# Optimization experiments

Hardware: AMD Instinct MI355X
Metric: run time of the kernel (lower is better)

## Reference

```python
import jax, jax.numpy as jnp
import numpy as np

D = 1024
T = 32768


def setup_inputs() -> dict:
    key = jax.random.key(0)
    k1, k2, k3 = jax.random.split(key, 3)
    r_star = jax.random.normal(k1, (D,), dtype=jnp.float32)
    q_t = jax.random.normal(k2, (T, D), dtype=jnp.float32)
    W = jax.random.normal(k3, (D,), dtype=jnp.float32) * (2.0 / D) ** 0.5  # ~GlorotNormal
    b = jnp.zeros((1,), dtype=jnp.float32)
    return {"r_star": r_star, "q_t": q_t, "W": W, "b": b}


def reference(r_star, q_t, W, b):
    # beta_stars[t] = W * (r_star * q_t[t]) + b  -> [T, D]
    beta = W[None, :] * (r_star[None, :] * q_t) + b  # fused elementwise
    # tf.nn.softmax default axis=-1 (over D)
    alpha = jax.nn.softmax(beta, axis=-1)  # [T, D]
    # weighted sum over the T axis -> [D]
    q_t_star = jnp.sum(alpha * q_t, axis=0)
    return q_t_star
```

## Files before the change

### kernel.cpp

```cpp
#include <hip/hip_runtime.h>
#include <math.h>

constexpr int D_   = 1024;
constexpr int T_   = 32768;
constexpr int TPB  = 1024;
constexpr int WPB  = TPB / 64;
constexpr int NBLK = 256;
constexpr int TOTW = NBLK * WPB;
constexpr int ROWS = T_ / TOTW;
constexpr int NC4  = D_ / 4;

typedef float f32x4 __attribute__((ext_vector_type(4)));

__global__ __launch_bounds__(TPB) void attn_pass1_fixed(
    const float* __restrict__ r_star,
    const float* __restrict__ q_t,
    const float* __restrict__ W,
    float* __restrict__ partialT)
{
    __shared__ f32x4 lds4[WPB * NC4];

    const int tid  = threadIdx.x;
    const int lane = tid & 63;
    const int wv   = tid >> 6;
    const int gw   = blockIdx.x * WPB + wv;

    constexpr float LOG2E = 1.4426950408889634f;

    const f32x4* r4 = reinterpret_cast<const f32x4*>(r_star);
    const f32x4* w4 = reinterpret_cast<const f32x4*>(W);
    f32x4 s[4];
#pragma unroll
    for (int k = 0; k < 4; ++k)
        s[k] = r4[lane + 64 * k] * w4[lane + 64 * k] * LOG2E;

    f32x4 acc[4];
#pragma unroll
    for (int k = 0; k < 4; ++k) acc[k] = (f32x4)(0.f);

    const f32x4* qb = reinterpret_cast<const f32x4*>(q_t);
    size_t off = (size_t)gw * NC4 + lane;
    constexpr size_t STR = (size_t)TOTW * NC4;

    for (int i = 0; i < ROWS; ++i) {
        f32x4 q[4];
#pragma unroll
        for (int k = 0; k < 4; ++k) q[k] = qb[off + 64 * k];
        off += STR;

        f32x4 bb[4];
#pragma unroll
        for (int k = 0; k < 4; ++k) {
            const f32x4 t = s[k] * q[k];
            bb[k].x = exp2f(t.x);
            bb[k].y = exp2f(t.y);
            bb[k].z = exp2f(t.z);
            bb[k].w = exp2f(t.w);
        }
        const float s0 = ((bb[0].x + bb[0].y) + (bb[0].z + bb[0].w))
                       + ((bb[1].x + bb[1].y) + (bb[1].z + bb[1].w));
        const float s1 = ((bb[2].x + bb[2].y) + (bb[2].z + bb[2].w))
                       + ((bb[3].x + bb[3].y) + (bb[3].z + bb[3].w));
        float ssum = s0 + s1;
#pragma unroll
        for (int o = 32; o > 0; o >>= 1)
            ssum += __shfl_xor(ssum, o, 64);

        const float inv = __builtin_amdgcn_rcpf(ssum);
#pragma unroll
        for (int k = 0; k < 4; ++k) {
            const f32x4 a = bb[k] * inv;
            acc[k].x = fmaf(a.x, q[k].x, acc[k].x);
            acc[k].y = fmaf(a.y, q[k].y, acc[k].y);
            acc[k].z = fmaf(a.z, q[k].z, acc[k].z);
            acc[k].w = fmaf(a.w, q[k].w, acc[k].w);
        }
    }

#pragma unroll
    for (int k = 0; k < 4; ++k) lds4[wv * NC4 + lane + 64 * k] = acc[k];
    __syncthreads();
    if (tid < NC4) {
        f32x4 sum = lds4[tid];
#pragma unroll
        for (int w = 1; w < WPB; ++w) sum += lds4[w * NC4 + tid];
        reinterpret_cast<f32x4*>(partialT)[(size_t)tid * NBLK + blockIdx.x] = sum;
    }
}

__global__ __launch_bounds__(256) void attn_pass2t(
    const float* __restrict__ partialT,
    float* __restrict__ out)
{
    __shared__ f32x4 red[256];
    const int tid = threadIdx.x;
    const int c   = blockIdx.x;
    red[tid] = reinterpret_cast<const f32x4*>(partialT)[(size_t)c * NBLK + tid];
    __syncthreads();
#pragma unroll
    for (int s = 128; s >= 1; s >>= 1) {
        if (tid < s) red[tid] += red[tid + s];
        __syncthreads();
    }
    if (tid == 0)
        reinterpret_cast<f32x4*>(out)[c] = red[0];
}

__global__ __launch_bounds__(512) void attn_pass1_generic(
    const float* __restrict__ r_star,
    const float* __restrict__ q_t,
    const float* __restrict__ W,
    float* __restrict__ partial)
{
    __shared__ f32x4 lds4[8 * NC4];
    const int tid  = threadIdx.x;
    const int lane = tid & 63;
    const int wv   = tid >> 6;
    const int totalWaves = gridDim.x * 8;
    const int gw = blockIdx.x * 8 + wv;
    constexpr float LOG2E = 1.4426950408889634f;

    const f32x4* r4 = reinterpret_cast<const f32x4*>(r_star);
    const f32x4* w4 = reinterpret_cast<const f32x4*>(W);
    f32x4 s[4];
#pragma unroll
    for (int k = 0; k < 4; ++k)
        s[k] = r4[lane + 64 * k] * w4[lane + 64 * k] * LOG2E;
    f32x4 acc[4];
#pragma unroll
    for (int k = 0; k < 4; ++k) acc[k] = (f32x4)(0.f);

    for (int t = gw; t < T_; t += totalWaves) {
        const f32x4* qrow = reinterpret_cast<const f32x4*>(q_t) + (size_t)t * NC4;
        f32x4 q[4];
#pragma unroll
        for (int k = 0; k < 4; ++k) q[k] = qrow[lane + 64 * k];
        f32x4 bb[4];
        float ssum = 0.f;
#pragma unroll
        for (int k = 0; k < 4; ++k) {
            const f32x4 tt = s[k] * q[k];
            bb[k].x = exp2f(tt.x); bb[k].y = exp2f(tt.y);
            bb[k].z = exp2f(tt.z); bb[k].w = exp2f(tt.w);
            ssum += (bb[k].x + bb[k].y) + (bb[k].z + bb[k].w);
        }
#pragma unroll
        for (int o = 32; o > 0; o >>= 1) ssum += __shfl_xor(ssum, o, 64);
        const float inv = __builtin_amdgcn_rcpf(ssum);
#pragma unroll
        for (int k = 0; k < 4; ++k) {
            const f32x4 a = bb[k] * inv;
            acc[k].x = fmaf(a.x, q[k].x, acc[k].x);
            acc[k].y = fmaf(a.y, q[k].y, acc[k].y);
            acc[k].z = fmaf(a.z, q[k].z, acc[k].z);
            acc[k].w = fmaf(a.w, q[k].w, acc[k].w);
        }
    }
#pragma unroll
    for (int k = 0; k < 4; ++k) lds4[wv * NC4 + lane + 64 * k] = acc[k];
    __syncthreads();
    if (tid < NC4) {
        f32x4 sum = lds4[tid];
        for (int w = 1; w < 8; ++w) sum += lds4[w * NC4 + tid];
        reinterpret_cast<f32x4*>(partial)[(size_t)blockIdx.x * NC4 + tid] = sum;
    }
}

__global__ __launch_bounds__(256) void attn_pass2_lin(
    const float* __restrict__ partial,
    float* __restrict__ out, int nblk)
{
    __shared__ f32x4 red[256];
    const int tid = threadIdx.x;
    const int f4  = tid & 3;
    const int bg  = tid >> 2;
    const int d4b = blockIdx.x * 4;
    const f32x4* p4 = reinterpret_cast<const f32x4*>(partial);

    f32x4 acc = (f32x4)(0.f);
    for (int b = bg; b < nblk; b += 64)
        acc += p4[(size_t)b * NC4 + d4b + f4];
    red[tid] = acc;
    __syncthreads();
#pragma unroll
    for (int s = 128; s >= 4; s >>= 1) {
        if (tid < s) red[tid] += red[tid + s];
        __syncthreads();
    }
    if (tid < 4)
        reinterpret_cast<f32x4*>(out)[d4b + tid] = red[tid];
}

extern "C" void kernel_launch(void* const* d_in, const int* in_sizes, int n_in,
                              void* d_out, int out_size, void* d_ws, size_t ws_size,
                              hipStream_t stream) {
    const float* r_star = (const float*)d_in[0];
    const float* q_t    = (const float*)d_in[1];
    const float* W      = (const float*)d_in[2];
    float* out     = (float*)d_out;
    float* partial = (float*)d_ws;

    const size_t need = (size_t)NBLK * D_ * sizeof(float);
    if (ws_size >= need) {
        attn_pass1_fixed<<<NBLK, TPB, 0, stream>>>(r_star, q_t, W, partial);
        attn_pass2t<<<NC4, 256, 0, stream>>>(partial, out);
    } else {
        int nblk = (int)(ws_size / ((size_t)D_ * sizeof(float)));
        if (nblk < 1) nblk = 1;
        attn_pass1_generic<<<nblk, 512, 0, stream>>>(r_star, q_t, W, partial);
        attn_pass2_lin<<<D_ / 16, 256, 0, stream>>>(partial, out, nblk);
    }
}
```

Baseline: 29.59 us.

## Fuse both reduction passes into one cooperative kernel with grid sync

```diff
diff --git a/kernel.cpp b/kernel.cpp
--- a/kernel.cpp
+++ b/kernel.cpp
@@ -1,4 +1,5 @@
 #include <hip/hip_runtime.h>
+#include <hip/hip_cooperative_groups.h>
 #include <math.h>
 
 constexpr int D_   = 1024;
@@ -12,6 +13,97 @@
 
 typedef float f32x4 __attribute__((ext_vector_type(4)));
 
+__global__ __launch_bounds__(TPB) void attn_fused(
+    const float* __restrict__ r_star,
+    const float* __restrict__ q_t,
+    const float* __restrict__ W,
+    float* __restrict__ partialT,
+    float* __restrict__ out)
+{
+    __shared__ f32x4 lds4[WPB * NC4];
+
+    const int tid  = threadIdx.x;
+    const int lane = tid & 63;
+    const int wv   = tid >> 6;
+    const int gw   = blockIdx.x * WPB + wv;
+
+    constexpr float LOG2E = 1.4426950408889634f;
+
+    const f32x4* r4 = reinterpret_cast<const f32x4*>(r_star);
+    const f32x4* w4 = reinterpret_cast<const f32x4*>(W);
+    f32x4 s[4];
+#pragma unroll
+    for (int k = 0; k < 4; ++k)
+        s[k] = r4[lane + 64 * k] * w4[lane + 64 * k] * LOG2E;
+
+    f32x4 acc[4];
+#pragma unroll
+    for (int k = 0; k < 4; ++k) acc[k] = (f32x4)(0.f);
+
+    const f32x4* qb = reinterpret_cast<const f32x4*>(q_t);
+    size_t off = (size_t)gw * NC4 + lane;
+    constexpr size_t STR = (size_t)TOTW * NC4;
+
+    for (int i = 0; i < ROWS; ++i) {
+        f32x4 q[4];
+#pragma unroll
+        for (int k = 0; k < 4; ++k) q[k] = qb[off + 64 * k];
+        off += STR;
+
+        f32x4 bb[4];
+#pragma unroll
+        for (int k = 0; k < 4; ++k) {
+            const f32x4 t = s[k] * q[k];
+            bb[k].x = exp2f(t.x);
+            bb[k].y = exp2f(t.y);
+            bb[k].z = exp2f(t.z);
+            bb[k].w = exp2f(t.w);
+        }
+        const float s0 = ((bb[0].x + bb[0].y) + (bb[0].z + bb[0].w))
+                       + ((bb[1].x + bb[1].y) + (bb[1].z + bb[1].w));
+        const float s1 = ((bb[2].x + bb[2].y) + (bb[2].z + bb[2].w))
+                       + ((bb[3].x + bb[3].y) + (bb[3].z + bb[3].w));
+        float ssum = s0 + s1;
+#pragma unroll
+        for (int o = 32; o > 0; o >>= 1)
+            ssum += __shfl_xor(ssum, o, 64);
+
+        const float inv = __builtin_amdgcn_rcpf(ssum);
+#pragma unroll
+        for (int k = 0; k < 4; ++k) {
+            const f32x4 a = bb[k] * inv;
+            acc[k].x = fmaf(a.x, q[k].x, acc[k].x);
+            acc[k].y = fmaf(a.y, q[k].y, acc[k].y);
+            acc[k].z = fmaf(a.z, q[k].z, acc[k].z);
+            acc[k].w = fmaf(a.w, q[k].w, acc[k].w);
+        }
+    }
+
+#pragma unroll
+    for (int k = 0; k < 4; ++k) lds4[wv * NC4 + lane + 64 * k] = acc[k];
+    __syncthreads();
+    if (tid < NC4) {
+        f32x4 sum = lds4[tid];
+#pragma unroll
+        for (int w = 1; w < WPB; ++w) sum += lds4[w * NC4 + tid];
+        reinterpret_cast<f32x4*>(partialT)[(size_t)tid * NBLK + blockIdx.x] = sum;
+    }
+
+    cooperative_groups::this_grid().sync();
+
+    const int c = blockIdx.x;
+    if (tid < NBLK)
+        lds4[tid] = reinterpret_cast<const f32x4*>(partialT)[(size_t)c * NBLK + tid];
+    __syncthreads();
+#pragma unroll
+    for (int sh = NBLK / 2; sh >= 1; sh >>= 1) {
+        if (tid < sh) lds4[tid] += lds4[tid + sh];
+        __syncthreads();
+    }
+    if (tid == 0)
+        reinterpret_cast<f32x4*>(out)[c] = lds4[0];
+}
+
 __global__ __launch_bounds__(TPB) void attn_pass1_fixed(
     const float* __restrict__ r_star,
     const float* __restrict__ q_t,
@@ -19,12 +111,10 @@
     float* __restrict__ partialT)
 {
     __shared__ f32x4 lds4[WPB * NC4];
-
     const int tid  = threadIdx.x;
     const int lane = tid & 63;
     const int wv   = tid >> 6;
     const int gw   = blockIdx.x * WPB + wv;
-
     constexpr float LOG2E = 1.4426950408889634f;
 
     const f32x4* r4 = reinterpret_cast<const f32x4*>(r_star);
@@ -33,7 +123,6 @@
 #pragma unroll
     for (int k = 0; k < 4; ++k)
         s[k] = r4[lane + 64 * k] * w4[lane + 64 * k] * LOG2E;
-
     f32x4 acc[4];
 #pragma unroll
     for (int k = 0; k < 4; ++k) acc[k] = (f32x4)(0.f);
@@ -47,15 +136,12 @@
 #pragma unroll
         for (int k = 0; k < 4; ++k) q[k] = qb[off + 64 * k];
         off += STR;
-
         f32x4 bb[4];
 #pragma unroll
         for (int k = 0; k < 4; ++k) {
             const f32x4 t = s[k] * q[k];
-            bb[k].x = exp2f(t.x);
-            bb[k].y = exp2f(t.y);
-            bb[k].z = exp2f(t.z);
-            bb[k].w = exp2f(t.w);
+            bb[k].x = exp2f(t.x); bb[k].y = exp2f(t.y);
+            bb[k].z = exp2f(t.z); bb[k].w = exp2f(t.w);
         }
         const float s0 = ((bb[0].x + bb[0].y) + (bb[0].z + bb[0].w))
                        + ((bb[1].x + bb[1].y) + (bb[1].z + bb[1].w));
@@ -65,7 +151,6 @@
 #pragma unroll
         for (int o = 32; o > 0; o >>= 1)
             ssum += __shfl_xor(ssum, o, 64);
-
         const float inv = __builtin_amdgcn_rcpf(ssum);
 #pragma unroll
         for (int k = 0; k < 4; ++k) {
@@ -76,7 +161,6 @@
             acc[k].w = fmaf(a.w, q[k].w, acc[k].w);
         }
     }
-
 #pragma unroll
     for (int k = 0; k < 4; ++k) lds4[wv * NC4 + lane + 64 * k] = acc[k];
     __syncthreads();
@@ -106,91 +190,6 @@
         reinterpret_cast<f32x4*>(out)[c] = red[0];
 }
 
-__global__ __launch_bounds__(512) void attn_pass1_generic(
-    const float* __restrict__ r_star,
-    const float* __restrict__ q_t,
-    const float* __restrict__ W,
-    float* __restrict__ partial)
-{
-    __shared__ f32x4 lds4[8 * NC4];
-    const int tid  = threadIdx.x;
-    const int lane = tid & 63;
-    const int wv   = tid >> 6;
-    const int totalWaves = gridDim.x * 8;
-    const int gw = blockIdx.x * 8 + wv;
-    constexpr float LOG2E = 1.4426950408889634f;
-
-    const f32x4* r4 = reinterpret_cast<const f32x4*>(r_star);
-    const f32x4* w4 = reinterpret_cast<const f32x4*>(W);
-    f32x4 s[4];
-#pragma unroll
-    for (int k = 0; k < 4; ++k)
-        s[k] = r4[lane + 64 * k] * w4[lane + 64 * k] * LOG2E;
-    f32x4 acc[4];
-#pragma unroll
-    for (int k = 0; k < 4; ++k) acc[k] = (f32x4)(0.f);
-
-    for (int t = gw; t < T_; t += totalWaves) {
-        const f32x4* qrow = reinterpret_cast<const f32x4*>(q_t) + (size_t)t * NC4;
-        f32x4 q[4];
-#pragma unroll
-        for (int k = 0; k < 4; ++k) q[k] = qrow[lane + 64 * k];
-        f32x4 bb[4];
-        float ssum = 0.f;
-#pragma unroll
-        for (int k = 0; k < 4; ++k) {
-            const f32x4 tt = s[k] * q[k];
-            bb[k].x = exp2f(tt.x); bb[k].y = exp2f(tt.y);
-            bb[k].z = exp2f(tt.z); bb[k].w = exp2f(tt.w);
-            ssum += (bb[k].x + bb[k].y) + (bb[k].z + bb[k].w);
-        }
-#pragma unroll
-        for (int o = 32; o > 0; o >>= 1) ssum += __shfl_xor(ssum, o, 64);
-        const float inv = __builtin_amdgcn_rcpf(ssum);
-#pragma unroll
-        for (int k = 0; k < 4; ++k) {
-            const f32x4 a = bb[k] * inv;
-            acc[k].x = fmaf(a.x, q[k].x, acc[k].x);
-            acc[k].y = fmaf(a.y, q[k].y, acc[k].y);
-            acc[k].z = fmaf(a.z, q[k].z, acc[k].z);
-            acc[k].w = fmaf(a.w, q[k].w, acc[k].w);
-        }
-    }
-#pragma unroll
-    for (int k = 0; k < 4; ++k) lds4[wv * NC4 + lane + 64 * k] = acc[k];
-    __syncthreads();
-    if (tid < NC4) {
-        f32x4 sum = lds4[tid];
-        for (int w = 1; w < 8; ++w) sum += lds4[w * NC4 + tid];
-        reinterpret_cast<f32x4*>(partial)[(size_t)blockIdx.x * NC4 + tid] = sum;
-    }
-}
-
-__global__ __launch_bounds__(256) void attn_pass2_lin(
-    const float* __restrict__ partial,
-    float* __restrict__ out, int nblk)
-{
-    __shared__ f32x4 red[256];
-    const int tid = threadIdx.x;
-    const int f4  = tid & 3;
-    const int bg  = tid >> 2;
-    const int d4b = blockIdx.x * 4;
-    const f32x4* p4 = reinterpret_cast<const f32x4*>(partial);
-
-    f32x4 acc = (f32x4)(0.f);
-    for (int b = bg; b < nblk; b += 64)
-        acc += p4[(size_t)b * NC4 + d4b + f4];
-    red[tid] = acc;
-    __syncthreads();
-#pragma unroll
-    for (int s = 128; s >= 4; s >>= 1) {
-        if (tid < s) red[tid] += red[tid + s];
-        __syncthreads();
-    }
-    if (tid < 4)
-        reinterpret_cast<f32x4*>(out)[d4b + tid] = red[tid];
-}
-
 extern "C" void kernel_launch(void* const* d_in, const int* in_sizes, int n_in,
                               void* d_out, int out_size, void* d_ws, size_t ws_size,
                               hipStream_t stream) {
@@ -200,14 +199,12 @@
     float* out     = (float*)d_out;
     float* partial = (float*)d_ws;
 
-    const size_t need = (size_t)NBLK * D_ * sizeof(float);
-    if (ws_size >= need) {
+    void* args[] = {(void*)&r_star, (void*)&q_t, (void*)&W,
+                    (void*)&partial, (void*)&out};
+    hipError_t err = hipLaunchCooperativeKernel(
+        (const void*)attn_fused, dim3(NBLK), dim3(TPB), args, 0, stream);
+    if (err != hipSuccess) {
         attn_pass1_fixed<<<NBLK, TPB, 0, stream>>>(r_star, q_t, W, partial);
         attn_pass2t<<<NC4, 256, 0, stream>>>(partial, out);
-    } else {
-        int nblk = (int)(ws_size / ((size_t)D_ * sizeof(float)));
-        if (nblk < 1) nblk = 1;
-        attn_pass1_generic<<<nblk, 512, 0, stream>>>(r_star, q_t, W, partial);
-        attn_pass2_lin<<<D_ / 16, 256, 0, stream>>>(partial, out, nblk);
-    }
-}
+    }
+}
```

After: 72.58 us. +145.3%, slower.
